# Optimization experiments

Hardware: AMD Instinct MI355X
Metric: run time of the kernel (lower is better)

## Reference

```python
import jax, jax.numpy as jnp
import numpy as np

WS = 7          # window size (7x7)
N = WS * WS     # tokens per window = 49
C = 192         # channels
H = 6           # heads
NW = 64         # windows per image (for mask)
B_ = 8192       # num_windows * batch


def _rel_index():
    coords = np.stack(np.meshgrid(np.arange(WS), np.arange(WS), indexing='ij'))  # [2,7,7]
    cf = coords.reshape(2, -1)                       # [2,49]
    rc = (cf[:, :, None] - cf[:, None, :]).transpose(1, 2, 0).astype(np.int64)  # [49,49,2]
    rc[..., 0] += WS - 1
    rc[..., 1] += WS - 1
    rc[..., 0] *= 2 * WS - 1
    return jnp.asarray(rc.sum(-1), dtype=jnp.int32)  # [49,49], values in [0, 169)


def setup_inputs() -> dict:
    key = jax.random.key(0)
    ks = jax.random.split(key, 10)
    std = 0.02
    return {
        'xq': jax.random.normal(ks[0], (B_, N, C), dtype=jnp.float32),
        'mask': jax.random.normal(ks[1], (NW, N, N), dtype=jnp.float32),
        'Wq': jax.random.normal(ks[2], (C, C), dtype=jnp.float32) * std,
        'bq': jnp.zeros((C,), dtype=jnp.float32),
        'Wkv': jax.random.normal(ks[3], (C, 2 * C), dtype=jnp.float32) * std,
        'bkv': jnp.zeros((2 * C,), dtype=jnp.float32),
        'Wproj': jax.random.normal(ks[4], (C, C), dtype=jnp.float32) * std,
        'bproj': jnp.zeros((C,), dtype=jnp.float32),
        'bias_table': jax.random.normal(ks[5], ((2 * WS - 1) * (2 * WS - 1), H), dtype=jnp.float32) * std,
        'rel_index': _rel_index(),
    }


def reference(xq, mask, Wq, bq, Wkv, bkv, Wproj, bproj, bias_table, rel_index):
    b_, n, c = xq.shape
    h = H
    dh = c // h
    scale = dh ** (-0.5)
    # projections (xkv = xq since xkv is None in the original call)
    q = (xq @ Wq + bq).reshape(b_, n, h, dh).transpose(0, 2, 1, 3) * scale      # [b_,h,n,dh]
    kv = (xq @ Wkv + bkv).reshape(b_, n, 2, h, dh).transpose(2, 0, 3, 1, 4)     # [2,b_,h,n,dh]
    k, v = kv[0], kv[1]
    attn = jnp.einsum('bhqd,bhkd->bhqk', q, k)                                   # [b_,h,n,n]
    # gathered relative-position bias: [n,n,h] -> [h,n,n]
    bias = bias_table[rel_index.reshape(-1)].reshape(n, n, h).transpose(2, 0, 1)
    attn = attn + bias[None]
    # mask add: [b_//nw, nw, h, n, n] + [1, nw, 1, n, n]
    nw = mask.shape[0]
    attn = attn.reshape(b_ // nw, nw, h, n, n) + mask[None, :, None]
    attn = jax.nn.softmax(attn.reshape(b_, h, n, n), axis=-1)
    x = jnp.einsum('bhqk,bhkd->bhqd', attn, v).transpose(0, 2, 1, 3).reshape(b_, n, c)
    return x @ Wproj + bproj
```

## Files before the change

kernel.cpp:

```cpp
#include <hip/hip_runtime.h>


#define NTOK 49
#define CCH 192
#define WPB 8

typedef __bf16 bf16_t;
typedef bf16_t bf16x8 __attribute__((ext_vector_type(8)));
typedef bf16_t bf16x4 __attribute__((ext_vector_type(4)));
typedef bf16_t bf16x2 __attribute__((ext_vector_type(2)));
typedef float f32x4 __attribute__((ext_vector_type(4)));

#define WS_WQT   0
#define WS_WKVT  73728
#define WS_WPT   221184
#define WS_BQS   294912
#define WS_TBL   295680
#define WS_QKV   5112576
#define QT_WIN   9408
#define VT_WIN   10752
#define QKV_BYTES_PER_WIN 59136

#define SWZ(row, off) ((off) ^ (((row) & 7) << 4))

__device__ __forceinline__ unsigned pk2(float a, float b) {
    bf16x2 w = { (bf16_t)a, (bf16_t)b };
    return __builtin_bit_cast(unsigned, w);
}

__global__ void prep_kernel(const float* __restrict__ Wq, const float* __restrict__ bq,
                            const float* __restrict__ Wkv, const float* __restrict__ Wproj,
                            const float* __restrict__ btab, const int* __restrict__ rel,
                            const float* __restrict__ mask,
                            bf16_t* __restrict__ wqt, bf16_t* __restrict__ wkvt,
                            bf16_t* __restrict__ wpt, float* __restrict__ bqs,
                            float* __restrict__ tbl, int mode) {
    const float SC  = 0.2550718212080052f;
    const float L2E = 1.4426950408889634f;
    long i = (long)blockIdx.x * 256 + threadIdx.x;
    if (i < 36864) { int n = i / 192, k = i % 192; wqt[i] = (bf16_t)(Wq[k * 192 + n] * SC); return; }
    i -= 36864;
    if (i < 73728) { int n = i / 192, k = i % 192; wkvt[i] = (bf16_t)Wkv[k * 384 + n]; return; }
    i -= 73728;
    if (i < 36864) { int n = i / 192, k = i % 192; wpt[i] = (bf16_t)Wproj[k * 192 + n]; return; }
    i -= 36864;
    if (i < 192) { bqs[i] = bq[i] * SC; return; }
    i -= 192;
    if (mode == 0) {
        if (i < 1204224) {
            int c = i & 63; long r = i >> 6; int q = r % 49; r /= 49; int h = r % 6; int w = r / 6;
            tbl[i] = (c < 49) ? (btab[rel[q * 49 + c] * 6 + h] + mask[(size_t)w * 2401 + q * 49 + c]) * L2E
                              : -1e30f;
        }
    } else if (mode == 1) {
        if (i < 18816) { int c = i & 63; int r = i >> 6; int q = r % 49; int h = r / 49;
            tbl[i] = (c < 49) ? btab[rel[q * 49 + c] * 6 + h] * L2E : 0.f; return; }
        i -= 18816;
        if (i < 200704) { int c = i & 63; long r = i >> 6; int q = r % 49; int w = r / 49;
            tbl[18816 + i] = (c < 49) ? mask[(size_t)w * 2401 + q * 49 + c] * L2E : -1e30f; }
    } else {
        if (i < 14406) { int h = i / 2401, rc = i % 2401; tbl[i] = btab[rel[rc] * 6 + h]; }
    }
}

__global__ __launch_bounds__(512) void qkv2_kernel(
    const float* __restrict__ xq, const float* __restrict__ bkv,
    const bf16_t* __restrict__ wqt, const bf16_t* __restrict__ wkvt,
    const float* __restrict__ bqs,
    bf16_t* __restrict__ qt, bf16_t* __restrict__ kt, bf16_t* __restrict__ vt,
    int base)
{
    __shared__ __align__(16) unsigned char Xs[24576];
    const int tid = threadIdx.x;
    const int wid = tid >> 6;
    const int lane = tid & 63;
    const int l15 = lane & 15;
    const int lg = lane >> 4;

    for (int i = 0; i < WPB; i++) {
        const int lw = blockIdx.x * WPB + i;
        const float* xp = xq + (size_t)(base + lw) * (NTOK * CCH);
        for (int idx = tid; idx < 2352; idx += 512) {
            int row = idx / 48, c4 = idx % 48;
            float4 v = *(const float4*)(xp + row * 192 + c4 * 4);
            bf16x4 pk = { (bf16_t)v.x, (bf16_t)v.y, (bf16_t)v.z, (bf16_t)v.w };
            *(bf16x4*)(Xs + row * 384 + SWZ(row, c4 * 8)) = pk;
        }
        for (int idx = tid; idx < 720; idx += 512)
            *(unsigned long long*)(Xs + 49 * 384 + idx * 8) = 0ULL;
        __syncthreads();

        const int ep = (lw & 3) << 1;
        for (int sp = 0; sp < 3; sp++) {
            int p;
            if (sp == 0) p = wid;
            else if (sp == 1) p = wid + 8;
            else if (wid == ep) p = 16;
            else if (wid == ep + 1) p = 17;
            else break;

            const int kind = (p < 6) ? 0 : (p < 12 ? 1 : 2);
            const int rp = (kind == 0) ? 0 : (kind == 1 ? 6 : 12);
            const int c0 = (p - rp) * 32;
            const int c1 = c0 + 16;
            const int rt = 2 * (p - rp);
            const bf16_t* w0;
            const bf16_t* w1;
            if (kind == 0) {
                w0 = wqt + (size_t)(c0 + l15) * 192 + lg * 8;
                w1 = wqt + (size_t)(c1 + l15) * 192 + lg * 8;
            } else {
                int ofs = (kind == 2) ? 192 : 0;
                w0 = wkvt + (size_t)(ofs + c0 + l15) * 192 + lg * 8;
                w1 = wkvt + (size_t)(ofs + c1 + l15) * 192 + lg * 8;
            }
            bf16x8 b0[6], b1[6];
#pragma unroll
            for (int ks = 0; ks < 6; ks++) {
                b0[ks] = *(const bf16x8*)(w0 + ks * 32);
                b1[ks] = *(const bf16x8*)(w1 + ks * 32);
            }
            if (kind < 2) {
                const float* bp = (kind == 0) ? bqs : bkv;
                float4 q0 = *(const float4*)(bp + c0 + lg * 4);
                float4 q1 = *(const float4*)(bp + c1 + lg * 4);
                bf16_t* dbase = (kind == 0) ? qt : kt;
                bf16_t* d0 = dbase + ((size_t)lw * 12 + rt) * 784;
                bf16_t* d1 = d0 + 784;
#pragma unroll
                for (int mt = 0; mt < 4; mt++) {
                    int xr = mt * 16 + l15;
                    bf16x8 xf[6];
#pragma unroll
                    for (int ks = 0; ks < 6; ks++)
                        xf[ks] = *(const bf16x8*)(Xs + xr * 384 + SWZ(xr, ks * 64 + lg * 16));
                    f32x4 a0 = { q0.x, q0.y, q0.z, q0.w };
                    f32x4 a1 = { q1.x, q1.y, q1.z, q1.w };
#pragma unroll
                    for (int ks = 0; ks < 6; ks++) {
                        a0 = __builtin_amdgcn_mfma_f32_16x16x32_bf16(b0[ks], xf[ks], a0, 0, 0, 0);
                        a1 = __builtin_amdgcn_mfma_f32_16x16x32_bf16(b1[ks], xf[ks], a1, 0, 0, 0);
                    }
                    int tok = mt * 16 + l15;
                    if (tok < NTOK) {
                        bf16x4 s0 = { (bf16_t)a0[0], (bf16_t)a0[1], (bf16_t)a0[2], (bf16_t)a0[3] };
                        bf16x4 s1 = { (bf16_t)a1[0], (bf16_t)a1[1], (bf16_t)a1[2], (bf16_t)a1[3] };
                        *(bf16x4*)(d0 + tok * 16 + lg * 4) = s0;
                        *(bf16x4*)(d1 + tok * 16 + lg * 4) = s1;
                    }
                }
            } else {
                float v0b = bkv[192 + c0 + l15];
                float v1b = bkv[192 + c1 + l15];
                bf16_t* e0 = vt + ((size_t)lw * 192 + c0 + l15) * 56;
                bf16_t* e1 = vt + ((size_t)lw * 192 + c1 + l15) * 56;
#pragma unroll
                for (int mt = 0; mt < 4; mt++) {
                    int xr = mt * 16 + l15;
                    bf16x8 xf[6];
#pragma unroll
                    for (int ks = 0; ks < 6; ks++)
                        xf[ks] = *(const bf16x8*)(Xs + xr * 384 + SWZ(xr, ks * 64 + lg * 16));
                    f32x4 a0 = { v0b, v0b, v0b, v0b };
                    f32x4 a1 = { v1b, v1b, v1b, v1b };
#pragma unroll
                    for (int ks = 0; ks < 6; ks++) {
                        a0 = __builtin_amdgcn_mfma_f32_16x16x32_bf16(xf[ks], b0[ks], a0, 0, 0, 0);
                        a1 = __builtin_amdgcn_mfma_f32_16x16x32_bf16(xf[ks], b1[ks], a1, 0, 0, 0);
                    }
                    int t0 = mt * 16 + lg * 4;
                    if (t0 < NTOK) {
                        bf16x4 s0 = { (bf16_t)a0[0], (bf16_t)a0[1], (bf16_t)a0[2], (bf16_t)a0[3] };
                        bf16x4 s1 = { (bf16_t)a1[0], (bf16_t)a1[1], (bf16_t)a1[2], (bf16_t)a1[3] };
                        *(bf16x4*)(e0 + t0) = s0;
                        *(bf16x4*)(e1 + t0) = s1;
                    }
                }
            }
        }
        __syncthreads();
    }
}

__global__ __launch_bounds__(512, 4) void attn2_kernel(
    const bf16_t* __restrict__ qt, const bf16_t* __restrict__ kt, const bf16_t* __restrict__ vt,
    const bf16_t* __restrict__ wpt, const float* __restrict__ bproj,
    const float* __restrict__ tbl, float* __restrict__ out, int base)
{
    __shared__ __align__(16) unsigned char smem[73728];
    unsigned char* Ks = smem;
    unsigned char* Vt = smem + 24576;
    unsigned char* Os = smem + 49152;

    const int tid = threadIdx.x;
    const int wid = tid >> 6;
    const int lane = tid & 63;
    const int l15 = lane & 15;
    const int lg = lane >> 4;
    const int t0i = blockIdx.x;
    const int bl = (t0i & ~63) | ((t0i & 7) << 3) | ((t0i >> 3) & 7);
    const int b = base + bl;
    const int widx = b & 63;

    const bf16_t* kg = kt + (size_t)bl * QT_WIN;
    const bf16_t* vg = vt + (size_t)bl * VT_WIN;
    const bf16_t* qg = qt + (size_t)bl * QT_WIN;

    for (int idx = tid; idx < 1176; idx += 512) {
        int t = idx / 24, c8 = idx % 24;
        bf16x8 v = *(const bf16x8*)(kg + ((size_t)(c8 >> 1) * 49 + t) * 16 + (c8 & 1) * 8);
        *(bf16x8*)(Ks + t * 384 + SWZ(t, c8 * 16)) = v;
    }
    for (int idx = tid; idx < 720; idx += 512)
        *(unsigned long long*)(Ks + 49 * 384 + idx * 8) = 0ULL;
    uint4 zz = { 0u, 0u, 0u, 0u };
    const bf16x8 z8 = __builtin_bit_cast(bf16x8, zz);
    for (int idx = tid; idx < 1536; idx += 512) {
        int ch = idx >> 3, c = idx & 7;
        bf16x8 v;
        if (c < 6) v = *(const bf16x8*)(vg + (size_t)ch * 56 + c * 8);
        else if (c == 6) {
            bf16x8 r = *(const bf16x8*)(vg + (size_t)ch * 56 + 48);
            v = z8; v[0] = r[0];
        } else v = z8;
        *(bf16x8*)(Vt + ch * 128 + SWZ(ch, c * 16)) = v;
    }
    bf16x8 qf[3];
#pragma unroll
    for (int i3 = 0; i3 < 3; i3++) {
        int u = wid + 8 * i3, h = u >> 2, qtl = u & 3;
        int qrow = qtl * 16 + l15;
        qf[i3] = (qrow < NTOK)
            ? *(const bf16x8*)(qg + ((size_t)(h * 2 + (lg >> 1)) * 49 + qrow) * 16 + (lg & 1) * 8)
            : z8;
    }
    float4 tb0[4], tb1[4];
    auto tload = [&](int i3, float4* dst) {
        int u = wid + 8 * i3, h = u >> 2, qtl = u & 3;
        int q = qtl * 16 + l15;
        if (q < NTOK) {
            const float* tp = tbl + (((size_t)(widx * 6 + h) * 49 + q) << 6) + lg * 4;
#pragma unroll
            for (int f = 0; f < 4; f++) dst[f] = *(const float4*)(tp + f * 16);
        } else {
#pragma unroll
            for (int f = 0; f < 4; f++) dst[f] = make_float4(0.f, 0.f, 0.f, 0.f);
        }
    };
    tload(0, tb0);
    __syncthreads();

#pragma unroll
    for (int i3 = 0; i3 < 3; i3++) {
        int u = wid + 8 * i3;
        int h = u >> 2, qtl = u & 3;
        bf16x8 qfr = qf[i3];
        if (i3 < 2) tload(i3 + 1, (i3 & 1) ? tb0 : tb1);
        f32x4 s[4];
#pragma unroll
        for (int f = 0; f < 4; f++) {
            int kr = f * 16 + l15;
            bf16x8 kfr = *(const bf16x8*)(Ks + kr * 384 + SWZ(kr, h * 64 + lg * 16));
            f32x4 z = { 0.f, 0.f, 0.f, 0.f };
            s[f] = __builtin_amdgcn_mfma_f32_16x16x32_bf16(kfr, qfr, z, 0, 0, 0);
        }
        int q = qtl * 16 + l15;
        bool qok = (q < NTOK);
        const float4* tbc = (i3 & 1) ? tb1 : tb0;
#pragma unroll
        for (int f = 0; f < 4; f++) {
            if (qok) {
                s[f][0] += tbc[f].x; s[f][1] += tbc[f].y; s[f][2] += tbc[f].z; s[f][3] += tbc[f].w;
            } else {
#pragma unroll
                for (int j = 0; j < 4; j++) { int k = f * 16 + lg * 4 + j; if (k >= NTOK) s[f][j] = -1e30f; }
            }
        }
        float m = s[0][0];
#pragma unroll
        for (int f = 0; f < 4; f++)
#pragma unroll
            for (int j = 0; j < 4; j++) m = fmaxf(m, s[f][j]);
        m = fmaxf(m, __shfl_xor(m, 16));
        m = fmaxf(m, __shfl_xor(m, 32));
        float t = 0.f;
#pragma unroll
        for (int f = 0; f < 4; f++)
#pragma unroll
            for (int j = 0; j < 4; j++) { s[f][j] = __builtin_amdgcn_exp2f(s[f][j] - m); t += s[f][j]; }
        t += __shfl_xor(t, 16);
        t += __shfl_xor(t, 32);
        float inv = __builtin_amdgcn_rcpf(t);
        unsigned Wp[8];
#pragma unroll
        for (int f = 0; f < 4; f++) {
            Wp[f * 2 + 0] = pk2(s[f][0], s[f][1]);
            Wp[f * 2 + 1] = pk2(s[f][2], s[f][3]);
        }
        bf16x8 pa[2];
#pragma unroll
        for (int ks2 = 0; ks2 < 2; ks2++) {
            unsigned pw[4];
#pragma unroll
            for (int p = 0; p < 4; p++) {
                int src = l15 + 16 * (((lg & 1) << 1) | (p >> 1));
                unsigned v0 = (unsigned)__shfl((int)Wp[(2 * ks2) * 2 + (p & 1)], src, 64);
                unsigned v1 = (unsigned)__shfl((int)Wp[(2 * ks2 + 1) * 2 + (p & 1)], src, 64);
                pw[p] = (lg & 2) ? v1 : v0;
            }
            uint4 pp = { pw[0], pw[1], pw[2], pw[3] };
            pa[ks2] = __builtin_bit_cast(bf16x8, pp);
        }
#pragma unroll
        for (int dt = 0; dt < 2; dt++) {
            f32x4 acc = { 0.f, 0.f, 0.f, 0.f };
#pragma unroll
            for (int ks2 = 0; ks2 < 2; ks2++) {
                int vr = h * 32 + dt * 16 + l15;
                bf16x8 vfr = *(const bf16x8*)(Vt + vr * 128 + SWZ(vr, ks2 * 64 + lg * 16));
                acc = __builtin_amdgcn_mfma_f32_16x16x32_bf16(vfr, pa[ks2], acc, 0, 0, 0);
            }
            int orow = qtl * 16 + l15;
            bf16x4 op4 = { (bf16_t)(acc[0] * inv), (bf16_t)(acc[1] * inv),
                           (bf16_t)(acc[2] * inv), (bf16_t)(acc[3] * inv) };
            *(bf16x4*)(Os + orow * 384 + SWZ(orow, h * 64 + dt * 32 + lg * 8)) = op4;
        }
    }
    __syncthreads();

    {
        float* op = out + (size_t)b * (NTOK * CCH);
        bf16x8 bfr[6];
        float4 b4 = { 0.f, 0.f, 0.f, 0.f };
        int prev_nt = -1;
        for (int i = 0; i < 6; i++) {
            int u = wid * 6 + i;
            int nt = u >> 2, mt = u & 3;
            if (nt != prev_nt) {
                prev_nt = nt;
                const bf16_t* wr = wpt + (size_t)(nt * 16 + l15) * 192 + lg * 8;
#pragma unroll
                for (int ks = 0; ks < 6; ks++) bfr[ks] = *(const bf16x8*)(wr + ks * 32);
                b4 = *(const float4*)(bproj + nt * 16 + lg * 4);
            }
            int orow = mt * 16 + l15;
            f32x4 acc = { b4.x, b4.y, b4.z, b4.w };
#pragma unroll
            for (int ks = 0; ks < 6; ks++) {
                bf16x8 of = *(const bf16x8*)(Os + orow * 384 + SWZ(orow, ks * 64 + lg * 16));
                acc = __builtin_amdgcn_mfma_f32_16x16x32_bf16(bfr[ks], of, acc, 0, 0, 0);
            }
            if (orow < NTOK) {
                float4 st = { acc[0], acc[1], acc[2], acc[3] };
                *(float4*)(op + orow * 192 + nt * 16 + lg * 4) = st;
            }
        }
    }
}

__global__ __launch_bounds__(512, 4) void wattn_mono(
    const float* __restrict__ xq, const float* __restrict__ mask,
    const float* __restrict__ bkv, const float* __restrict__ bproj,
    const bf16_t* __restrict__ wqt, const bf16_t* __restrict__ wkvt, const bf16_t* __restrict__ wpt,
    const float* __restrict__ bqs, const float* __restrict__ tbl,
    float* __restrict__ out, int mode)
{
    __shared__ __align__(16) unsigned char smem[73728];
    unsigned char* QsO = smem;
    unsigned char* Ks  = smem + 24576;
    unsigned char* Vt  = smem + 49152;

    const int tid = threadIdx.x;
    const int wid = tid >> 6;
    const int lane = tid & 63;
    const int l15 = lane & 15;
    const int lg = lane >> 4;
    const int t0 = blockIdx.x;
    const int b = (t0 & 0x1FC0) | ((t0 & 7) << 3) | ((t0 >> 3) & 7);
    const float* xp = xq + (size_t)b * (NTOK * CCH);
    const float LOG2E = 1.4426950408889634f;

    const int mtp = wid & 1;
    const int ntq = wid >> 1;
    bf16x8 xf[2][6];
#pragma unroll
    for (int e = 0; e < 2; e++) {
        int tok = (mtp * 2 + e) * 16 + l15;
        const float* xrow = xp + (size_t)tok * 192;
        bool ok = (tok < NTOK);
#pragma unroll
        for (int ks = 0; ks < 6; ks++) {
            float4 a = { 0.f, 0.f, 0.f, 0.f }, c = { 0.f, 0.f, 0.f, 0.f };
            if (ok) {
                a = *(const float4*)(xrow + ks * 32 + lg * 8);
                c = *(const float4*)(xrow + ks * 32 + lg * 8 + 4);
            }
            bf16x8 f = { (bf16_t)a.x, (bf16_t)a.y, (bf16_t)a.z, (bf16_t)a.w,
                         (bf16_t)c.x, (bf16_t)c.y, (bf16_t)c.z, (bf16_t)c.w };
            xf[e][ks] = f;
        }
    }
    for (int k9 = 0; k9 < 9; k9++) {
        int nt = ntq + 4 * k9;
        int kind = nt < 12 ? 0 : (nt < 24 ? 1 : 2);
        int ncol = (nt - (kind == 1 ? 12 : (kind == 2 ? 24 : 0))) * 16;
        const bf16_t* wr;
        if (kind == 0)      wr = wqt  + (size_t)(ncol + l15) * 192 + lg * 8;
        else if (kind == 1) wr = wkvt + (size_t)(ncol + l15) * 192 + lg * 8;
        else                wr = wkvt + (size_t)(192 + ncol + l15) * 192 + lg * 8;
        bf16x8 bfr[6];
#pragma unroll
        for (int ks = 0; ks < 6; ks++) bfr[ks] = *(const bf16x8*)(wr + ks * 32);
        if (kind < 2) {
            float4 b4 = (kind == 0) ? *(const float4*)(bqs + ncol + lg * 4)
                                    : *(const float4*)(bkv + ncol + lg * 4);
            f32x4 acc0 = { b4.x, b4.y, b4.z, b4.w }, acc1 = acc0;
#pragma unroll
            for (int ks = 0; ks < 6; ks++) {
                acc0 = __builtin_amdgcn_mfma_f32_16x16x32_bf16(bfr[ks], xf[0][ks], acc0, 0, 0, 0);
                acc1 = __builtin_amdgcn_mfma_f32_16x16x32_bf16(bfr[ks], xf[1][ks], acc1, 0, 0, 0);
            }
            unsigned char* dst = (kind == 0) ? QsO : Ks;
            int tr0 = (mtp * 2) * 16 + l15;
            int tr1 = tr0 + 16;
            bf16x4 p0 = { (bf16_t)acc0[0], (bf16_t)acc0[1], (bf16_t)acc0[2], (bf16_t)acc0[3] };
            bf16x4 p1 = { (bf16_t)acc1[0], (bf16_t)acc1[1], (bf16_t)acc1[2], (bf16_t)acc1[3] };
            *(bf16x4*)(dst + tr0 * 384 + SWZ(tr0, ncol * 2 + lg * 8)) = p0;
            *(bf16x4*)(dst + tr1 * 384 + SWZ(tr1, ncol * 2 + lg * 8)) = p1;
        } else {
            float bv = bkv[192 + ncol + l15];
            f32x4 acc0 = { bv, bv, bv, bv }, acc1 = acc0;
#pragma unroll
            for (int ks = 0; ks < 6; ks++) {
                acc0 = __builtin_amdgcn_mfma_f32_16x16x32_bf16(xf[0][ks], bfr[ks], acc0, 0, 0, 0);
                acc1 = __builtin_amdgcn_mfma_f32_16x16x32_bf16(xf[1][ks], bfr[ks], acc1, 0, 0, 0);
            }
            int vr = ncol + l15;
            bf16x4 v0 = { (bf16_t)acc0[0], (bf16_t)acc0[1], (bf16_t)acc0[2], (bf16_t)acc0[3] };
            bf16x4 v1 = { (bf16_t)acc1[0], (bf16_t)acc1[1], (bf16_t)acc1[2], (bf16_t)acc1[3] };
            *(bf16x4*)(Vt + vr * 128 + SWZ(vr, (mtp * 2) * 32 + lg * 8)) = v0;
            *(bf16x4*)(Vt + vr * 128 + SWZ(vr, (mtp * 2 + 1) * 32 + lg * 8)) = v1;
        }
    }
    __syncthreads();

    const int widx = b & 63;
    for (int i3 = 0; i3 < 3; i3++) {
        int u = wid + 8 * i3;
        int h = u >> 2, qtl = u & 3;
        int qrow = qtl * 16 + l15;
        bf16x8 qfr = *(const bf16x8*)(QsO + qrow * 384 + SWZ(qrow, h * 64 + lg * 16));
        f32x4 s[4];
#pragma unroll
        for (int f = 0; f < 4; f++) {
            int kr = f * 16 + l15;
            bf16x8 kfr = *(const bf16x8*)(Ks + kr * 384 + SWZ(kr, h * 64 + lg * 16));
            f32x4 z = { 0.f, 0.f, 0.f, 0.f };
            s[f] = __builtin_amdgcn_mfma_f32_16x16x32_bf16(kfr, qfr, z, 0, 0, 0);
        }
        int q = qtl * 16 + l15;
        bool qok = (q < NTOK);
        if (mode == 0) {
#pragma unroll
            for (int f = 0; f < 4; f++) {
                if (qok) {
                    float4 bm = *(const float4*)(tbl + (((size_t)(widx * 6 + h) * 49 + q) << 6) + f * 16 + lg * 4);
                    s[f][0] += bm.x; s[f][1] += bm.y; s[f][2] += bm.z; s[f][3] += bm.w;
                } else {
#pragma unroll
                    for (int j = 0; j < 4; j++) { int k = f * 16 + lg * 4 + j; if (k >= NTOK) s[f][j] = -1e30f; }
                }
            }
        } else if (mode == 1) {
#pragma unroll
            for (int f = 0; f < 4; f++) {
                if (qok) {
                    float4 b1 = *(const float4*)(tbl + (((size_t)(h * 49 + q)) << 6) + f * 16 + lg * 4);
                    float4 m1 = *(const float4*)(tbl + 18816 + (((size_t)(widx * 49 + q)) << 6) + f * 16 + lg * 4);
                    s[f][0] += b1.x + m1.x; s[f][1] += b1.y + m1.y;
                    s[f][2] += b1.z + m1.z; s[f][3] += b1.w + m1.w;
                } else {
#pragma unroll
                    for (int j = 0; j < 4; j++) { int k = f * 16 + lg * 4 + j; if (k >= NTOK) s[f][j] = -1e30f; }
                }
            }
        } else {
#pragma unroll
            for (int f = 0; f < 4; f++)
#pragma unroll
                for (int j = 0; j < 4; j++) {
                    int k = f * 16 + lg * 4 + j;
                    if (k >= NTOK) s[f][j] = -1e30f;
                    else if (qok)
                        s[f][j] += (tbl[h * 2401 + q * 49 + k] + mask[(size_t)widx * 2401 + q * 49 + k]) * LOG2E;
                }
        }
        float m = s[0][0];
#pragma unroll
        for (int f = 0; f < 4; f++)
#pragma unroll
            for (int j = 0; j < 4; j++) m = fmaxf(m, s[f][j]);
        m = fmaxf(m, __shfl_xor(m, 16));
        m = fmaxf(m, __shfl_xor(m, 32));
        float t = 0.f;
#pragma unroll
        for (int f = 0; f < 4; f++)
#pragma unroll
            for (int j = 0; j < 4; j++) { s[f][j] = __builtin_amdgcn_exp2f(s[f][j] - m); t += s[f][j]; }
        t += __shfl_xor(t, 16);
        t += __shfl_xor(t, 32);
        float inv = __builtin_amdgcn_rcpf(t);
        unsigned Wp[8];
#pragma unroll
        for (int f = 0; f < 4; f++) {
            Wp[f * 2 + 0] = pk2(s[f][0], s[f][1]);
            Wp[f * 2 + 1] = pk2(s[f][2], s[f][3]);
        }
        bf16x8 pa[2];
#pragma unroll
        for (int ks2 = 0; ks2 < 2; ks2++) {
            unsigned pw[4];
#pragma unroll
            for (int p = 0; p < 4; p++) {
                int src = l15 + 16 * (((lg & 1) << 1) | (p >> 1));
                unsigned v0 = (unsigned)__shfl((int)Wp[(2 * ks2) * 2 + (p & 1)], src, 64);
                unsigned v1 = (unsigned)__shfl((int)Wp[(2 * ks2 + 1) * 2 + (p & 1)], src, 64);
                pw[p] = (lg & 2) ? v1 : v0;
            }
            uint4 pp = { pw[0], pw[1], pw[2], pw[3] };
            pa[ks2] = __builtin_bit_cast(bf16x8, pp);
        }
#pragma unroll
        for (int dt = 0; dt < 2; dt++) {
            f32x4 acc = { 0.f, 0.f, 0.f, 0.f };
#pragma unroll
            for (int ks2 = 0; ks2 < 2; ks2++) {
                int vr = h * 32 + dt * 16 + l15;
                bf16x8 vfr = *(const bf16x8*)(Vt + vr * 128 + SWZ(vr, ks2 * 64 + lg * 16));
                acc = __builtin_amdgcn_mfma_f32_16x16x32_bf16(vfr, pa[ks2], acc, 0, 0, 0);
            }
            int orow = qtl * 16 + l15;
            bf16x4 op4 = { (bf16_t)(acc[0] * inv), (bf16_t)(acc[1] * inv),
                           (bf16_t)(acc[2] * inv), (bf16_t)(acc[3] * inv) };
            *(bf16x4*)(QsO + orow * 384 + SWZ(orow, h * 64 + dt * 32 + lg * 8)) = op4;
        }
    }
    __syncthreads();

    {
        float* op = out + (size_t)b * (NTOK * CCH);
        bf16x8 bfr[6];
        float4 b4 = { 0.f, 0.f, 0.f, 0.f };
        int prev_nt = -1;
        for (int i = 0; i < 6; i++) {
            int u = wid * 6 + i;
            int nt = u >> 2, mt = u & 3;
            if (nt != prev_nt) {
                prev_nt = nt;
                const bf16_t* wr = wpt + (size_t)(nt * 16 + l15) * 192 + lg * 8;
#pragma unroll
                for (int ks = 0; ks < 6; ks++) bfr[ks] = *(const bf16x8*)(wr + ks * 32);
                b4 = *(const float4*)(bproj + nt * 16 + lg * 4);
            }
            int orow = mt * 16 + l15;
            f32x4 acc = { b4.x, b4.y, b4.z, b4.w };
#pragma unroll
            for (int ks = 0; ks < 6; ks++) {
                bf16x8 of = *(const bf16x8*)(QsO + orow * 384 + SWZ(orow, ks * 64 + lg * 16));
                acc = __builtin_amdgcn_mfma_f32_16x16x32_bf16(bfr[ks], of, acc, 0, 0, 0);
            }
            if (orow < NTOK) {
                float4 st = { acc[0], acc[1], acc[2], acc[3] };
                *(float4*)(op + orow * 192 + nt * 16 + lg * 4) = st;
            }
        }
    }
}

extern "C" void kernel_launch(void* const* d_in, const int* in_sizes, int n_in,
                              void* d_out, int out_size, void* d_ws, size_t ws_size,
                              hipStream_t stream) {
    const float* xq    = (const float*)d_in[0];
    const float* mask  = (const float*)d_in[1];
    const float* Wq    = (const float*)d_in[2];
    const float* bq    = (const float*)d_in[3];
    const float* Wkv   = (const float*)d_in[4];
    const float* bkv   = (const float*)d_in[5];
    const float* Wproj = (const float*)d_in[6];
    const float* bproj = (const float*)d_in[7];
    const float* btab  = (const float*)d_in[8];
    const int*   rel   = (const int*)d_in[9];
    float* out = (float*)d_out;

    char* ws = (char*)d_ws;
    bf16_t* wqt  = (bf16_t*)(ws + WS_WQT);
    bf16_t* wkvt = (bf16_t*)(ws + WS_WKVT);
    bf16_t* wpt  = (bf16_t*)(ws + WS_WPT);
    float*  bqs  = (float*)(ws + WS_BQS);
    float*  tbl  = (float*)(ws + WS_TBL);

    size_t need0 = (size_t)WS_TBL + 1204224u * 4u;
    size_t need1 = (size_t)WS_TBL + 219520u * 4u;
    int mode = (ws_size >= need0) ? 0 : (ws_size >= need1 ? 1 : 2);

    long tblN = (mode == 0) ? 1204224L : (mode == 1 ? 219520L : 14406L);
    long prep_elems = 147648L + tblN;
    int prep_blocks = (int)((prep_elems + 255) / 256);
    prep_kernel<<<prep_blocks, 256, 0, stream>>>(Wq, bq, Wkv, Wproj, btab, rel, mask,
                                                 wqt, wkvt, wpt, bqs, tbl, mode);

    size_t avail = (ws_size > (size_t)WS_QKV) ? ws_size - (size_t)WS_QKV : 0;
    long w_c_l = (long)(avail / QKV_BYTES_PER_WIN) & ~63L;
    int w_c = (int)(w_c_l > 8192 ? 8192 : w_c_l);

    if (w_c >= 64 && mode == 0) {
        bf16_t* qtb = (bf16_t*)(ws + WS_QKV);
        bf16_t* ktb = qtb + (size_t)w_c * QT_WIN;
        bf16_t* vtb = ktb + (size_t)w_c * QT_WIN;
        for (int base = 0; base < 8192; base += w_c) {
            int n = (8192 - base) < w_c ? (8192 - base) : w_c;
            qkv2_kernel<<<n / WPB, 512, 0, stream>>>(xq, bkv, wqt, wkvt, bqs, qtb, ktb, vtb, base);
            attn2_kernel<<<n, 512, 0, stream>>>(qtb, ktb, vtb, wpt, bproj, tbl, out, base);
        }
    } else {
        wattn_mono<<<8192, 512, 0, stream>>>(xq, mask, bkv, bproj, wqt, wkvt, wpt,
                                             bqs, tbl, out, mode);
    }
}
```

Baseline: 672.7 us.

## Double-buffer QKV projection input and balance work units across warps

Rewrites the QKV projection kernel to process windows in pairs with two LDS buffers. The next pair's fp32 input is prefetched into registers while the current pair is computed, then committed to LDS after a barrier. Work is split into 36 (column-pair, window) units spread as 5/4 per warp, replacing the uneven 2-or-3-pass schedule. The block count is halved (16 windows per block) and launch bounds request 4 blocks per CU. Costs are extra registers for the prefetch staging and more LDS per block.

```diff
diff --git a/kernel.cpp b/kernel.cpp
--- a/kernel.cpp
+++ b/kernel.cpp
@@ -3,7 +3,6 @@
 
 #define NTOK 49
 #define CCH 192
-#define WPB 8
 
 typedef __bf16 bf16_t;
 typedef bf16_t bf16x8 __attribute__((ext_vector_type(8)));
@@ -63,67 +62,100 @@
     }
 }
 
-__global__ __launch_bounds__(512) void qkv2_kernel(
+__global__ __launch_bounds__(512, 4) void qkv3_kernel(
     const float* __restrict__ xq, const float* __restrict__ bkv,
     const bf16_t* __restrict__ wqt, const bf16_t* __restrict__ wkvt,
     const float* __restrict__ bqs,
     bf16_t* __restrict__ qt, bf16_t* __restrict__ kt, bf16_t* __restrict__ vt,
     int base)
 {
-    __shared__ __align__(16) unsigned char Xs[24576];
+    __shared__ __align__(16) unsigned char Xs[2][24576];
     const int tid = threadIdx.x;
     const int wid = tid >> 6;
     const int lane = tid & 63;
     const int l15 = lane & 15;
     const int lg = lane >> 4;
-
-    for (int i = 0; i < WPB; i++) {
-        const int lw = blockIdx.x * WPB + i;
-        const float* xp = xq + (size_t)(base + lw) * (NTOK * CCH);
-        for (int idx = tid; idx < 2352; idx += 512) {
-            int row = idx / 48, c4 = idx % 48;
-            float4 v = *(const float4*)(xp + row * 192 + c4 * 4);
-            bf16x4 pk = { (bf16_t)v.x, (bf16_t)v.y, (bf16_t)v.z, (bf16_t)v.w };
-            *(bf16x4*)(Xs + row * 384 + SWZ(row, c4 * 8)) = pk;
-        }
-        for (int idx = tid; idx < 720; idx += 512)
-            *(unsigned long long*)(Xs + 49 * 384 + idx * 8) = 0ULL;
+    const int lw0 = blockIdx.x * 16;
+
+    bf16x4 st[10];
+    auto prefetch = [&](int ph) {
+#pragma unroll
+        for (int j = 0; j < 10; j++) {
+            int g = j * 512 + tid;
+            if (g < 4704) {
+                int win = g / 2352, rem = g % 2352, r = rem / 48, c4 = rem % 48;
+                const float* xp = xq + (size_t)(base + lw0 + 2 * ph + win) * 9408 + r * 192 + c4 * 4;
+                float4 v = *(const float4*)xp;
+                st[j] = bf16x4{ (bf16_t)v.x, (bf16_t)v.y, (bf16_t)v.z, (bf16_t)v.w };
+            }
+        }
+    };
+    auto commit = [&]() {
+#pragma unroll
+        for (int j = 0; j < 10; j++) {
+            int g = j * 512 + tid;
+            if (g < 4704) {
+                int win = g / 2352, rem = g % 2352, r = rem / 48, c4 = rem % 48;
+                *(bf16x4*)(Xs[win] + r * 384 + SWZ(r, c4 * 8)) = st[j];
+            }
+        }
+    };
+
+    prefetch(0);
+    for (int idx = tid; idx < 1440; idx += 512) {
+        int win = idx / 720, o = idx % 720;
+        *(unsigned long long*)(Xs[win] + 49 * 384 + o * 8) = 0ULL;
+    }
+    commit();
+
+    const int u0 = (wid < 4) ? 5 * wid : 20 + 4 * (wid - 4);
+    const int nu = (wid < 4) ? 5 : 4;
+
+    for (int ph = 0; ph < 8; ph++) {
         __syncthreads();
-
-        const int ep = (lw & 3) << 1;
-        for (int sp = 0; sp < 3; sp++) {
-            int p;
-            if (sp == 0) p = wid;
-            else if (sp == 1) p = wid + 8;
-            else if (wid == ep) p = 16;
-            else if (wid == ep + 1) p = 17;
-            else break;
-
-            const int kind = (p < 6) ? 0 : (p < 12 ? 1 : 2);
-            const int rp = (kind == 0) ? 0 : (kind == 1 ? 6 : 12);
-            const int c0 = (p - rp) * 32;
-            const int c1 = c0 + 16;
-            const int rt = 2 * (p - rp);
-            const bf16_t* w0;
-            const bf16_t* w1;
-            if (kind == 0) {
-                w0 = wqt + (size_t)(c0 + l15) * 192 + lg * 8;
-                w1 = wqt + (size_t)(c1 + l15) * 192 + lg * 8;
-            } else {
-                int ofs = (kind == 2) ? 192 : 0;
-                w0 = wkvt + (size_t)(ofs + c0 + l15) * 192 + lg * 8;
-                w1 = wkvt + (size_t)(ofs + c1 + l15) * 192 + lg * 8;
-            }
-            bf16x8 b0[6], b1[6];
-#pragma unroll
-            for (int ks = 0; ks < 6; ks++) {
-                b0[ks] = *(const bf16x8*)(w0 + ks * 32);
-                b1[ks] = *(const bf16x8*)(w1 + ks * 32);
-            }
+        if (ph < 7) prefetch(ph + 1);
+
+        int prevPair = -1;
+        bf16x8 b0[6], b1[6];
+        float4 q0 = {0.f,0.f,0.f,0.f}, q1 = {0.f,0.f,0.f,0.f};
+        float v0b = 0.f, v1b = 0.f;
+        int kind = 0, c0 = 0, rt = 0;
+        for (int iu = 0; iu < nu; iu++) {
+            int u = u0 + iu;
+            int pair = u >> 1, win = u & 1;
+            if (pair != prevPair) {
+                prevPair = pair;
+                kind = (pair < 6) ? 0 : (pair < 12 ? 1 : 2);
+                const int rp = (kind == 0) ? 0 : (kind == 1 ? 6 : 12);
+                c0 = (pair - rp) * 32;
+                rt = 2 * (pair - rp);
+                const bf16_t* w0p;
+                const bf16_t* w1p;
+                if (kind == 0) {
+                    w0p = wqt + (size_t)(c0 + l15) * 192 + lg * 8;
+                    w1p = wqt + (size_t)(c0 + 16 + l15) * 192 + lg * 8;
+                } else {
+                    int ofs = (kind == 2) ? 192 : 0;
+                    w0p = wkvt + (size_t)(ofs + c0 + l15) * 192 + lg * 8;
+                    w1p = wkvt + (size_t)(ofs + c0 + 16 + l15) * 192 + lg * 8;
+                }
+#pragma unroll
+                for (int ks = 0; ks < 6; ks++) {
+                    b0[ks] = *(const bf16x8*)(w0p + ks * 32);
+                    b1[ks] = *(const bf16x8*)(w1p + ks * 32);
+                }
+                if (kind < 2) {
+                    const float* bp = (kind == 0) ? bqs : bkv;
+                    q0 = *(const float4*)(bp + c0 + lg * 4);
+                    q1 = *(const float4*)(bp + c0 + 16 + lg * 4);
+                } else {
+                    v0b = bkv[192 + c0 + l15];
+                    v1b = bkv[192 + c0 + 16 + l15];
+                }
+            }
+            const int lw = lw0 + 2 * ph + win;
+            const unsigned char* Xw = Xs[win];
             if (kind < 2) {
-                const float* bp = (kind == 0) ? bqs : bkv;
-                float4 q0 = *(const float4*)(bp + c0 + lg * 4);
-                float4 q1 = *(const float4*)(bp + c1 + lg * 4);
                 bf16_t* dbase = (kind == 0) ? qt : kt;
                 bf16_t* d0 = dbase + ((size_t)lw * 12 + rt) * 784;
                 bf16_t* d1 = d0 + 784;
@@ -133,7 +165,7 @@
                     bf16x8 xf[6];
 #pragma unroll
                     for (int ks = 0; ks < 6; ks++)
-                        xf[ks] = *(const bf16x8*)(Xs + xr * 384 + SWZ(xr, ks * 64 + lg * 16));
+                        xf[ks] = *(const bf16x8*)(Xw + xr * 384 + SWZ(xr, ks * 64 + lg * 16));
                     f32x4 a0 = { q0.x, q0.y, q0.z, q0.w };
                     f32x4 a1 = { q1.x, q1.y, q1.z, q1.w };
 #pragma unroll
@@ -150,17 +182,15 @@
                     }
                 }
             } else {
-                float v0b = bkv[192 + c0 + l15];
-                float v1b = bkv[192 + c1 + l15];
                 bf16_t* e0 = vt + ((size_t)lw * 192 + c0 + l15) * 56;
-                bf16_t* e1 = vt + ((size_t)lw * 192 + c1 + l15) * 56;
+                bf16_t* e1 = e0 + 16 * 56;
 #pragma unroll
                 for (int mt = 0; mt < 4; mt++) {
                     int xr = mt * 16 + l15;
                     bf16x8 xf[6];
 #pragma unroll
                     for (int ks = 0; ks < 6; ks++)
-                        xf[ks] = *(const bf16x8*)(Xs + xr * 384 + SWZ(xr, ks * 64 + lg * 16));
+                        xf[ks] = *(const bf16x8*)(Xw + xr * 384 + SWZ(xr, ks * 64 + lg * 16));
                     f32x4 a0 = { v0b, v0b, v0b, v0b };
                     f32x4 a1 = { v1b, v1b, v1b, v1b };
 #pragma unroll
@@ -178,7 +208,10 @@
                 }
             }
         }
-        __syncthreads();
+        if (ph < 7) {
+            __syncthreads();
+            commit();
+        }
     }
 }
 
@@ -619,7 +652,7 @@
         bf16_t* vtb = ktb + (size_t)w_c * QT_WIN;
         for (int base = 0; base < 8192; base += w_c) {
             int n = (8192 - base) < w_c ? (8192 - base) : w_c;
-            qkv2_kernel<<<n / WPB, 512, 0, stream>>>(xq, bkv, wqt, wkvt, bqs, qtb, ktb, vtb, base);
+            qkv3_kernel<<<n / 16, 512, 0, stream>>>(xq, bkv, wqt, wkvt, bqs, qtb, ktb, vtb, base);
             attn2_kernel<<<n, 512, 0, stream>>>(qtb, ktb, vtb, wpt, bproj, tbl, out, base);
         }
     } else {
```

New measurement: 658.9 us. -2.0%, faster.
